# Kernel tuning notes

Hardware: AMD Instinct MI355X
Metric: run time of the kernel (lower is better)

The kernel has to match this reference:

```python
import jax, jax.numpy as jnp
import numpy as np
import math

B, S, DIM = 2, 2048, 1024
H, D = 16, 64  # num_head, head_dim; H*D == DIM

def setup_inputs() -> dict:
    key = jax.random.key(0)
    ks = jax.random.split(key, 10)
    s = 0.02
    return {
        "X": jax.random.normal(ks[0], (B, S, DIM), dtype=jnp.float32),
        "mask": jnp.ones((B, S), dtype=jnp.float32),
        "Wq": jax.random.normal(ks[1], (DIM, H * D), dtype=jnp.float32) * s,
        "bq": jnp.zeros((H * D,), dtype=jnp.float32),
        "Wk": jax.random.normal(ks[2], (DIM, H * D), dtype=jnp.float32) * s,
        "bk": jnp.zeros((H * D,), dtype=jnp.float32),
        "Wv": jax.random.normal(ks[3], (DIM, H * D), dtype=jnp.float32) * s,
        "bv": jnp.zeros((H * D,), dtype=jnp.float32),
        "Wo": jax.random.normal(ks[4], (H * D, DIM), dtype=jnp.float32) * s,
        "bo": jnp.zeros((DIM,), dtype=jnp.float32),
    }

def _split_heads(x):
    # [B, S, H*D] -> [B, H, S, D]
    b, s, _ = x.shape
    return x.reshape(b, s, H, D).transpose(0, 2, 1, 3)

def reference(X, mask, Wq, bq, Wk, bk, Wv, bv, Wo, bo):
    Q = _split_heads(X @ Wq + bq)
    K = _split_heads(X @ Wk + bk)
    V = _split_heads(X @ Wv + bv)
    # scaled dot-product attention with additive mask penalty
    dot = jnp.einsum('bhqd,bhkd->bhqk', Q, K) / math.sqrt(D)
    dot = dot - 1e6 * (1.0 - mask[:, None, None, :])
    attn = jax.nn.softmax(dot, axis=-1)
    ctx = jnp.einsum('bhqk,bhkd->bhqd', attn, V)
    # combine heads: [B, H, S, D] -> [B, S, H*D]
    ctx = ctx.transpose(0, 2, 1, 3).reshape(B, S, H * D)
    return ctx @ Wo + bo
```

## Files before the change

kernel.cpp:

```cpp
#include <hip/hip_runtime.h>
#include <cstdint>
#include <cstddef>

typedef __attribute__((ext_vector_type(8))) _Float16 f16x8;
typedef __attribute__((ext_vector_type(4))) _Float16 f16x4;
typedef __attribute__((ext_vector_type(4))) float f32x4;

#define MFMA_16x16x32(a, b, c) __builtin_amdgcn_mfma_f32_16x16x32_f16((a), (b), (c), 0, 0, 0)
#define MFMA_16x16x16(a, b, c) __builtin_amdgcn_mfma_f32_16x16x16f16((a), (b), (c), 0, 0, 0)

static constexpr int kB = 2, kS = 2048, kDim = 1024, kH = 16, kD = 64;
static constexpr int kM = kB * kS;
static constexpr float kQScale = 0.125f * 1.44269504088896340736f;
static constexpr float kPenC = 1.44269504088896340736e6f;

__device__ __forceinline__ void wg_barrier_lds() {
  asm volatile("s_waitcnt lgkmcnt(0)" ::: "memory");
  __builtin_amdgcn_s_barrier();
}

__global__ void cvt_f32_to_f16(const float* __restrict__ in, _Float16* __restrict__ out, int n8) {
  int i = blockIdx.x * blockDim.x + threadIdx.x;
  if (i >= n8) return;
  const float4* p = (const float4*)in + (size_t)i * 2;
  float4 a = p[0], b = p[1];
  f16x8 h;
  h[0] = (_Float16)a.x; h[1] = (_Float16)a.y; h[2] = (_Float16)a.z; h[3] = (_Float16)a.w;
  h[4] = (_Float16)b.x; h[5] = (_Float16)b.y; h[6] = (_Float16)b.z; h[7] = (_Float16)b.w;
  ((f16x8*)out)[i] = h;
}

__global__ void transpose_cvt_w(const float* __restrict__ w0, const float* __restrict__ w1,
                                const float* __restrict__ w2, const float* __restrict__ w3,
                                _Float16* __restrict__ o0, _Float16* __restrict__ o1,
                                _Float16* __restrict__ o2, _Float16* __restrict__ o3) {
  const float* w; _Float16* o;
  switch (blockIdx.z) {
    case 0: w = w0; o = o0; break;
    case 1: w = w1; o = o1; break;
    case 2: w = w2; o = o2; break;
    default: w = w3; o = o3; break;
  }
  __shared__ alignas(16) _Float16 tile[64][72];
  const int kt = blockIdx.x * 64;
  const int nt = blockIdx.y * 64;
  const int tr = threadIdx.x >> 4;
  const int tc = threadIdx.x & 15;
#pragma unroll
  for (int rr = 0; rr < 4; ++rr) {
    int r = rr * 16 + tr;
    float4 v = *(const float4*)&w[(size_t)(kt + r) * kDim + nt + tc * 4];
    f16x4 hv;
    hv[0] = (_Float16)v.x; hv[1] = (_Float16)v.y; hv[2] = (_Float16)v.z; hv[3] = (_Float16)v.w;
    *(f16x4*)&tile[r][tc * 4] = hv;
  }
  __syncthreads();
#pragma unroll
  for (int rr = 0; rr < 4; ++rr) {
    int nl = rr * 16 + tr;
    f16x4 hv;
    hv[0] = tile[tc * 4 + 0][nl];
    hv[1] = tile[tc * 4 + 1][nl];
    hv[2] = tile[tc * 4 + 2][nl];
    hv[3] = tile[tc * 4 + 3][nl];
    *(f16x4*)&o[(size_t)(nt + nl) * kDim + kt + tc * 4] = hv;
  }
}

__global__ __launch_bounds__(256, 3) void gemm_qkv(
    const _Float16* __restrict__ A,
    const _Float16* __restrict__ wt0, const _Float16* __restrict__ wt1, const _Float16* __restrict__ wt2,
    const float* __restrict__ bias0, const float* __restrict__ bias1, const float* __restrict__ bias2,
    _Float16* __restrict__ oq, _Float16* __restrict__ ok, _Float16* __restrict__ ov) {
  const _Float16* Bt; const float* bias; _Float16* out;
  switch (blockIdx.z) {
    case 0: Bt = wt0; bias = bias0; out = oq; break;
    case 1: Bt = wt1; bias = bias1; out = ok; break;
    default: Bt = wt2; bias = bias2; out = ov; break;
  }
  __shared__ alignas(16) _Float16 As[2][128 * 40];
  __shared__ alignas(16) _Float16 Bs[2][128 * 40];
  const int tid = threadIdx.x;
  const int lane = tid & 63;
  const int wave = tid >> 6;
  const int wm = wave & 1, wn = wave >> 1;
  const int l15 = lane & 15, quad = lane >> 4;
  const int m0 = blockIdx.x * 128, n0 = blockIdx.y * 128;

  const int srow = tid >> 2;
  const int skc = (tid & 3) * 8;

  f32x4 acc[4][4] = {};
  f16x8 ra[2], rb[2];

#pragma unroll
  for (int i = 0; i < 2; ++i) {
    int row = srow + 64 * i;
    ra[i] = *(const f16x8*)&A[(size_t)(m0 + row) * kDim + skc];
    rb[i] = *(const f16x8*)&Bt[(size_t)(n0 + row) * kDim + skc];
  }
#pragma unroll
  for (int i = 0; i < 2; ++i) {
    int row = srow + 64 * i;
    *(f16x8*)&As[0][row * 40 + skc] = ra[i];
    *(f16x8*)&Bs[0][row * 40 + skc] = rb[i];
  }

  for (int kt = 0; kt < 32; ++kt) {
    const int cur = kt & 1;
    if (kt + 1 < 32) {
      int k0 = (kt + 1) * 32;
#pragma unroll
      for (int i = 0; i < 2; ++i) {
        int row = srow + 64 * i;
        ra[i] = *(const f16x8*)&A[(size_t)(m0 + row) * kDim + k0 + skc];
        rb[i] = *(const f16x8*)&Bt[(size_t)(n0 + row) * kDim + k0 + skc];
      }
    }
    wg_barrier_lds();
    {
      f16x8 af[4], bf[4];
#pragma unroll
      for (int t = 0; t < 4; ++t) af[t] = *(const f16x8*)&As[cur][(wm * 64 + t * 16 + l15) * 40 + quad * 8];
#pragma unroll
      for (int t = 0; t < 4; ++t) bf[t] = *(const f16x8*)&Bs[cur][(wn * 64 + t * 16 + l15) * 40 + quad * 8];
      __builtin_amdgcn_s_setprio(1);
#pragma unroll
      for (int i = 0; i < 4; ++i)
#pragma unroll
        for (int j = 0; j < 4; ++j)
          acc[i][j] = MFMA_16x16x32(af[i], bf[j], acc[i][j]);
      __builtin_amdgcn_s_setprio(0);
    }
    if (kt + 1 < 32) {
#pragma unroll
      for (int i = 0; i < 2; ++i) {
        int row = srow + 64 * i;
        *(f16x8*)&As[cur ^ 1][row * 40 + skc] = ra[i];
        *(f16x8*)&Bs[cur ^ 1][row * 40 + skc] = rb[i];
      }
    }
  }

  const int mbase = m0 + wm * 64 + quad * 4;
  const int nbase = n0 + wn * 64 + l15;
  if (blockIdx.z == 2) {
#pragma unroll
    for (int j = 0; j < 4; ++j) {
      int n = nbase + j * 16;
      float bv = bias[n];
      int h = n >> 6, d = n & 63;
#pragma unroll
      for (int i = 0; i < 4; ++i) {
        int m = mbase + i * 16;
        int b = m >> 11, s = m & (kS - 1);
        f16x4 hv;
#pragma unroll
        for (int r = 0; r < 4; ++r) hv[r] = (_Float16)(acc[i][j][r] + bv);
        *(f16x4*)&out[((size_t)((b * kH + h) * kD + d)) * kS + s] = hv;
      }
    }
  } else {
    const float osc = (blockIdx.z == 0) ? kQScale : 1.0f;
#pragma unroll
    for (int j = 0; j < 4; ++j) {
      int n = nbase + j * 16;
      float bv = bias[n];
      int h = n >> 6, d = n & 63;
#pragma unroll
      for (int i = 0; i < 4; ++i) {
        int mrow = mbase + i * 16;
#pragma unroll
        for (int r = 0; r < 4; ++r) {
          int m = mrow + r;
          int b = m >> 11, s = m & (kS - 1);
          out[(size_t)(((b * kH + h) * kS) + s) * kD + d] = (_Float16)((acc[i][j][r] + bv) * osc);
        }
      }
    }
  }
}

__global__ __launch_bounds__(256, 2) void attn(
    const _Float16* __restrict__ Q, const _Float16* __restrict__ K,
    const _Float16* __restrict__ V, const float* __restrict__ mask,
    _Float16* __restrict__ ctx) {
  const int id = blockIdx.x;
  const int logical = (id & 7) * 64 + (id >> 3);
  const int bh = logical >> 4;
  const int qblk = logical & 15;
  const int b = bh >> 4;
  const int q0 = qblk * 128;
  const int tid = threadIdx.x, lane = tid & 63, wave = tid >> 6;
  const int l15 = lane & 15, quad = lane >> 4;

  __shared__ alignas(16) _Float16 Ks[2][128 * 72];
  __shared__ alignas(16) _Float16 Vs[2][64 * 136];
  __shared__ alignas(16) float pens[kS];

  const _Float16* Qh = Q + (size_t)bh * kS * kD;
  const _Float16* Kh = K + (size_t)bh * kS * kD;
  const _Float16* Vh = V + (size_t)bh * kS * kD;

#pragma unroll
  for (int i = 0; i < 2; ++i) {
    float4 mv4 = *(const float4*)&mask[(size_t)b * kS + tid * 8 + i * 4];
    float4 pv;
    pv.x = (mv4.x - 1.0f) * kPenC;
    pv.y = (mv4.y - 1.0f) * kPenC;
    pv.z = (mv4.z - 1.0f) * kPenC;
    pv.w = (mv4.w - 1.0f) * kPenC;
    *(float4*)&pens[tid * 8 + i * 4] = pv;
  }

  f16x8 qf[2][2];
#pragma unroll
  for (int t = 0; t < 2; ++t) {
    int qrow = q0 + wave * 32 + t * 16 + l15;
#pragma unroll
    for (int kk = 0; kk < 2; ++kk)
      qf[t][kk] = *(const f16x8*)&Qh[(size_t)qrow * kD + kk * 32 + quad * 8];
  }

  f16x4 ones4;
#pragma unroll
  for (int i = 0; i < 4; ++i) ones4[i] = (_Float16)1.0f;

  f32x4 o_acc[2][4] = {};
  f32x4 l_acc[2] = {};

  const int srow = tid >> 3;
  const int skc = (tid & 7) * 8;
  const int vrow = tid >> 4;
  const int vcol = (tid & 15) * 8;

  f16x8 kreg[4], vreg[4];
#pragma unroll
  for (int i = 0; i < 4; ++i)
    kreg[i] = *(const f16x8*)&Kh[(size_t)(srow + 32 * i) * kD + skc];
#pragma unroll
  for (int i = 0; i < 4; ++i)
    vreg[i] = *(const f16x8*)&Vh[(size_t)(vrow + 16 * i) * kS + vcol];
#pragma unroll
  for (int i = 0; i < 4; ++i)
    *(f16x8*)&Ks[0][(srow + 32 * i) * 72 + skc] = kreg[i];
#pragma unroll
  for (int i = 0; i < 4; ++i)
    *(f16x8*)&Vs[0][(vrow + 16 * i) * 136 + vcol] = vreg[i];

  for (int it = 0; it < 16; ++it) {
    const int cur = it & 1;
    const int kb = it * 128;
    if (it + 1 < 16) {
#pragma unroll
      for (int i = 0; i < 4; ++i)
        kreg[i] = *(const f16x8*)&Kh[(size_t)(kb + 128 + srow + 32 * i) * kD + skc];
#pragma unroll
      for (int i = 0; i < 4; ++i)
        vreg[i] = *(const f16x8*)&Vh[(size_t)(vrow + 16 * i) * kS + kb + 128 + vcol];
    }
    wg_barrier_lds();

#pragma unroll
    for (int colt = 0; colt < 8; ++colt) {
      f32x4 pn = *(const f32x4*)&pens[kb + colt * 16 + quad * 4];
      f16x8 kf0 = *(const f16x8*)&Ks[cur][(colt * 16 + l15) * 72 + quad * 8];
      f16x8 kf1 = *(const f16x8*)&Ks[cur][(colt * 16 + l15) * 72 + 32 + quad * 8];
      f32x4 s0 = pn, s1 = pn;
      s0 = MFMA_16x16x32(kf0, qf[0][0], s0);
      s0 = MFMA_16x16x32(kf1, qf[0][1], s0);
      s1 = MFMA_16x16x32(kf0, qf[1][0], s1);
      s1 = MFMA_16x16x32(kf1, qf[1][1], s1);
      f16x4 vf0 = *(const f16x4*)&Vs[cur][(0 * 16 + l15) * 136 + colt * 16 + quad * 4];
      f16x4 vf1 = *(const f16x4*)&Vs[cur][(1 * 16 + l15) * 136 + colt * 16 + quad * 4];
      f16x4 vf2 = *(const f16x4*)&Vs[cur][(2 * 16 + l15) * 136 + colt * 16 + quad * 4];
      f16x4 vf3 = *(const f16x4*)&Vs[cur][(3 * 16 + l15) * 136 + colt * 16 + quad * 4];
      f16x4 pa0, pa1;
#pragma unroll
      for (int r = 0; r < 4; ++r) {
        pa0[r] = (_Float16)__builtin_exp2f(s0[r]);
        pa1[r] = (_Float16)__builtin_exp2f(s1[r]);
      }
      __builtin_amdgcn_s_setprio(1);
      o_acc[0][0] = MFMA_16x16x16(pa0, vf0, o_acc[0][0]);
      o_acc[0][1] = MFMA_16x16x16(pa0, vf1, o_acc[0][1]);
      o_acc[0][2] = MFMA_16x16x16(pa0, vf2, o_acc[0][2]);
      o_acc[0][3] = MFMA_16x16x16(pa0, vf3, o_acc[0][3]);
      o_acc[1][0] = MFMA_16x16x16(pa1, vf0, o_acc[1][0]);
      o_acc[1][1] = MFMA_16x16x16(pa1, vf1, o_acc[1][1]);
      o_acc[1][2] = MFMA_16x16x16(pa1, vf2, o_acc[1][2]);
      o_acc[1][3] = MFMA_16x16x16(pa1, vf3, o_acc[1][3]);
      l_acc[0] = MFMA_16x16x16(pa0, ones4, l_acc[0]);
      l_acc[1] = MFMA_16x16x16(pa1, ones4, l_acc[1]);
      __builtin_amdgcn_s_setprio(0);
    }

    if (it + 1 < 16) {
#pragma unroll
      for (int i = 0; i < 4; ++i)
        *(f16x8*)&Ks[cur ^ 1][(srow + 32 * i) * 72 + skc] = kreg[i];
#pragma unroll
      for (int i = 0; i < 4; ++i)
        *(f16x8*)&Vs[cur ^ 1][(vrow + 16 * i) * 136 + vcol] = vreg[i];
    }
  }

  const int h = bh & 15;
#pragma unroll
  for (int t = 0; t < 2; ++t) {
    f32x4 linv;
#pragma unroll
    for (int r = 0; r < 4; ++r) linv[r] = 1.0f / l_acc[t][r];
    int qbase = q0 + wave * 32 + t * 16 + quad * 4;
#pragma unroll
    for (int c = 0; c < 4; ++c) {
#pragma unroll
      for (int r = 0; r < 4; ++r) {
        ctx[((size_t)(b * kS + qbase + r)) * kDim + h * kD + c * 16 + l15] =
            (_Float16)(o_acc[t][c][r] * linv[r]);
      }
    }
  }
}

__global__ __launch_bounds__(256, 2) void gemm_out(
    const _Float16* __restrict__ A, const _Float16* __restrict__ Bt,
    const float* __restrict__ bias, float* __restrict__ out) {
  __shared__ alignas(16) _Float16 As[2][64 * 72];
  __shared__ alignas(16) _Float16 Bs[2][128 * 72];
  const int tid = threadIdx.x;
  const int lane = tid & 63;
  const int wave = tid >> 6;
  const int wm = wave & 1, wn = wave >> 1;
  const int l15 = lane & 15, quad = lane >> 4;
  const int m0 = blockIdx.x * 64, n0 = blockIdx.y * 128;

  const int srow = tid >> 3;
  const int skc = (tid & 7) * 8;

  f32x4 acc[2][4] = {};
  f16x8 ra[2], rb[4];

#pragma unroll
  for (int i = 0; i < 2; ++i)
    ra[i] = *(const f16x8*)&A[(size_t)(m0 + srow + 32 * i) * kDim + skc];
#pragma unroll
  for (int i = 0; i < 4; ++i)
    rb[i] = *(const f16x8*)&Bt[(size_t)(n0 + srow + 32 * i) * kDim + skc];
#pragma unroll
  for (int i = 0; i < 2; ++i)
    *(f16x8*)&As[0][(srow + 32 * i) * 72 + skc] = ra[i];
#pragma unroll
  for (int i = 0; i < 4; ++i)
    *(f16x8*)&Bs[0][(srow + 32 * i) * 72 + skc] = rb[i];

  for (int kt = 0; kt < 16; ++kt) {
    const int cur = kt & 1;
    if (kt + 1 < 16) {
      int k0 = (kt + 1) * 64;
#pragma unroll
      for (int i = 0; i < 2; ++i)
        ra[i] = *(const f16x8*)&A[(size_t)(m0 + srow + 32 * i) * kDim + k0 + skc];
#pragma unroll
      for (int i = 0; i < 4; ++i)
        rb[i] = *(const f16x8*)&Bt[(size_t)(n0 + srow + 32 * i) * kDim + k0 + skc];
    }
    wg_barrier_lds();
#pragma unroll
    for (int kk = 0; kk < 2; ++kk) {
      f16x8 af[2], bf[4];
#pragma unroll
      for (int t = 0; t < 2; ++t) af[t] = *(const f16x8*)&As[cur][(wm * 32 + t * 16 + l15) * 72 + kk * 32 + quad * 8];
#pragma unroll
      for (int t = 0; t < 4; ++t) bf[t] = *(const f16x8*)&Bs[cur][(wn * 64 + t * 16 + l15) * 72 + kk * 32 + quad * 8];
      __builtin_amdgcn_s_setprio(1);
#pragma unroll
      for (int i = 0; i < 2; ++i)
#pragma unroll
        for (int j = 0; j < 4; ++j)
          acc[i][j] = MFMA_16x16x32(af[i], bf[j], acc[i][j]);
      __builtin_amdgcn_s_setprio(0);
    }
    if (kt + 1 < 16) {
#pragma unroll
      for (int i = 0; i < 2; ++i)
        *(f16x8*)&As[cur ^ 1][(srow + 32 * i) * 72 + skc] = ra[i];
#pragma unroll
      for (int i = 0; i < 4; ++i)
        *(f16x8*)&Bs[cur ^ 1][(srow + 32 * i) * 72 + skc] = rb[i];
    }
  }

  const int mbase = m0 + wm * 32 + quad * 4;
  const int nbase = n0 + wn * 64 + l15;
#pragma unroll
  for (int j = 0; j < 4; ++j) {
    int n = nbase + j * 16;
    float bv = bias[n];
#pragma unroll
    for (int i = 0; i < 2; ++i) {
      int mrow = mbase + i * 16;
#pragma unroll
      for (int r = 0; r < 4; ++r)
        out[(size_t)(mrow + r) * kDim + n] = acc[i][j][r] + bv;
    }
  }
}

extern "C" void kernel_launch(void* const* d_in, const int* in_sizes, int n_in,
                              void* d_out, int out_size, void* d_ws, size_t ws_size,
                              hipStream_t stream) {
  (void)in_sizes; (void)n_in; (void)out_size; (void)ws_size;
  const float* X    = (const float*)d_in[0];
  const float* mask = (const float*)d_in[1];
  const float* Wq   = (const float*)d_in[2];
  const float* bq   = (const float*)d_in[3];
  const float* Wk   = (const float*)d_in[4];
  const float* bk   = (const float*)d_in[5];
  const float* Wv   = (const float*)d_in[6];
  const float* bv   = (const float*)d_in[7];
  const float* Wo   = (const float*)d_in[8];
  const float* bo   = (const float*)d_in[9];
  float* out = (float*)d_out;

  char* ws = (char*)d_ws;
  _Float16* Xh   = (_Float16*)(ws);
  _Float16* Wqt  = (_Float16*)(ws + ((size_t)8  << 20));
  _Float16* Wkt  = (_Float16*)(ws + ((size_t)10 << 20));
  _Float16* Wvt  = (_Float16*)(ws + ((size_t)12 << 20));
  _Float16* Wot  = (_Float16*)(ws + ((size_t)14 << 20));
  _Float16* Qh   = (_Float16*)(ws + ((size_t)16 << 20));
  _Float16* Kh   = (_Float16*)(ws + ((size_t)24 << 20));
  _Float16* Vh   = (_Float16*)(ws + ((size_t)32 << 20));
  _Float16* Ch   = (_Float16*)(ws + ((size_t)40 << 20));

  cvt_f32_to_f16<<<dim3(kM * kDim / 8 / 256), dim3(256), 0, stream>>>(X, Xh, kM * kDim / 8);
  transpose_cvt_w<<<dim3(16, 16, 4), dim3(256), 0, stream>>>(Wq, Wk, Wv, Wo, Wqt, Wkt, Wvt, Wot);
  gemm_qkv<<<dim3(32, 8, 3), dim3(256), 0, stream>>>(Xh, Wqt, Wkt, Wvt, bq, bk, bv, Qh, Kh, Vh);
  attn<<<dim3(512), dim3(256), 0, stream>>>(Qh, Kh, Vh, mask, Ch);
  gemm_out<<<dim3(64, 8), dim3(256), 0, stream>>>(Ch, Wot, bo, out);
}
```

Measured before the change: 199.7 us.

## Use direct global-to-LDS loads with XOR swizzle in projection GEMMs

```diff
diff --git a/kernel.cpp b/kernel.cpp
--- a/kernel.cpp
+++ b/kernel.cpp
@@ -17,6 +17,14 @@
 __device__ __forceinline__ void wg_barrier_lds() {
   asm volatile("s_waitcnt lgkmcnt(0)" ::: "memory");
   __builtin_amdgcn_s_barrier();
+}
+__device__ __forceinline__ void wg_barrier_vm() {
+  asm volatile("s_waitcnt vmcnt(0) lgkmcnt(0)" ::: "memory");
+  __builtin_amdgcn_s_barrier();
+}
+__device__ __forceinline__ void gload16(const void* g, void* l) {
+  __builtin_amdgcn_global_load_lds((const __attribute__((address_space(1))) void*)g,
+                                   (__attribute__((address_space(3))) void*)l, 16, 0, 0);
 }
 
 __global__ void cvt_f32_to_f16(const float* __restrict__ in, _Float16* __restrict__ out, int n8) {
@@ -67,7 +75,7 @@
   }
 }
 
-__global__ __launch_bounds__(256, 3) void gemm_qkv(
+__global__ __launch_bounds__(256, 2) void gemm_qkv(
     const _Float16* __restrict__ A,
     const _Float16* __restrict__ wt0, const _Float16* __restrict__ wt1, const _Float16* __restrict__ wt2,
     const float* __restrict__ bias0, const float* __restrict__ bias1, const float* __restrict__ bias2,
@@ -78,8 +86,8 @@
     case 1: Bt = wt1; bias = bias1; out = ok; break;
     default: Bt = wt2; bias = bias2; out = ov; break;
   }
-  __shared__ alignas(16) _Float16 As[2][128 * 40];
-  __shared__ alignas(16) _Float16 Bs[2][128 * 40];
+  __shared__ alignas(16) _Float16 As[2][128 * 64];
+  __shared__ alignas(16) _Float16 Bs[2][128 * 64];
   const int tid = threadIdx.x;
   const int lane = tid & 63;
   const int wave = tid >> 6;
@@ -87,43 +95,43 @@
   const int l15 = lane & 15, quad = lane >> 4;
   const int m0 = blockIdx.x * 128, n0 = blockIdx.y * 128;
 
-  const int srow = tid >> 2;
-  const int skc = (tid & 3) * 8;
+  const int grow = lane >> 3;
+  const int gcol = ((lane & 7) ^ grow) * 8;
+  const _Float16* Asrc = A  + (size_t)(m0 + wave * 32 + grow) * kDim + gcol;
+  const _Float16* Bsrc = Bt + (size_t)(n0 + wave * 32 + grow) * kDim + gcol;
+
+  const int xr = l15 & 7;
+  const int slotA0 = ((quad) ^ xr) * 16, slotA1 = ((4 + quad) ^ xr) * 16;
+  const int rbaseA = (wm * 64 + l15) * 128;
+  const int rbaseB = (wn * 64 + l15) * 128;
 
   f32x4 acc[4][4] = {};
-  f16x8 ra[2], rb[2];
-
-#pragma unroll
-  for (int i = 0; i < 2; ++i) {
-    int row = srow + 64 * i;
-    ra[i] = *(const f16x8*)&A[(size_t)(m0 + row) * kDim + skc];
-    rb[i] = *(const f16x8*)&Bt[(size_t)(n0 + row) * kDim + skc];
-  }
-#pragma unroll
-  for (int i = 0; i < 2; ++i) {
-    int row = srow + 64 * i;
-    *(f16x8*)&As[0][row * 40 + skc] = ra[i];
-    *(f16x8*)&Bs[0][row * 40 + skc] = rb[i];
-  }
-
-  for (int kt = 0; kt < 32; ++kt) {
+
+#pragma unroll
+  for (int g = 0; g < 4; ++g) {
+    gload16(Asrc + (size_t)g * 8 * kDim, (char*)&As[0][0] + (wave * 32 + g * 8) * 128);
+    gload16(Bsrc + (size_t)g * 8 * kDim, (char*)&Bs[0][0] + (wave * 32 + g * 8) * 128);
+  }
+  wg_barrier_vm();
+
+  for (int kt = 0; kt < 16; ++kt) {
     const int cur = kt & 1;
-    if (kt + 1 < 32) {
-      int k0 = (kt + 1) * 32;
-#pragma unroll
-      for (int i = 0; i < 2; ++i) {
-        int row = srow + 64 * i;
-        ra[i] = *(const f16x8*)&A[(size_t)(m0 + row) * kDim + k0 + skc];
-        rb[i] = *(const f16x8*)&Bt[(size_t)(n0 + row) * kDim + k0 + skc];
+    if (kt + 1 < 16) {
+      int koff = (kt + 1) * 64;
+#pragma unroll
+      for (int g = 0; g < 4; ++g) {
+        gload16(Asrc + (size_t)g * 8 * kDim + koff, (char*)&As[cur ^ 1][0] + (wave * 32 + g * 8) * 128);
+        gload16(Bsrc + (size_t)g * 8 * kDim + koff, (char*)&Bs[cur ^ 1][0] + (wave * 32 + g * 8) * 128);
       }
     }
-    wg_barrier_lds();
-    {
+#pragma unroll
+    for (int kk = 0; kk < 2; ++kk) {
+      const int sa = kk ? slotA1 : slotA0;
       f16x8 af[4], bf[4];
 #pragma unroll
-      for (int t = 0; t < 4; ++t) af[t] = *(const f16x8*)&As[cur][(wm * 64 + t * 16 + l15) * 40 + quad * 8];
-#pragma unroll
-      for (int t = 0; t < 4; ++t) bf[t] = *(const f16x8*)&Bs[cur][(wn * 64 + t * 16 + l15) * 40 + quad * 8];
+      for (int t = 0; t < 4; ++t) af[t] = *(const f16x8*)((const char*)&As[cur][0] + rbaseA + t * 2048 + sa);
+#pragma unroll
+      for (int t = 0; t < 4; ++t) bf[t] = *(const f16x8*)((const char*)&Bs[cur][0] + rbaseB + t * 2048 + sa);
       __builtin_amdgcn_s_setprio(1);
 #pragma unroll
       for (int i = 0; i < 4; ++i)
@@ -132,14 +140,7 @@
           acc[i][j] = MFMA_16x16x32(af[i], bf[j], acc[i][j]);
       __builtin_amdgcn_s_setprio(0);
     }
-    if (kt + 1 < 32) {
-#pragma unroll
-      for (int i = 0; i < 2; ++i) {
-        int row = srow + 64 * i;
-        *(f16x8*)&As[cur ^ 1][row * 40 + skc] = ra[i];
-        *(f16x8*)&Bs[cur ^ 1][row * 40 + skc] = rb[i];
-      }
-    }
+    if (kt + 1 < 16) wg_barrier_vm();
   }
 
   const int mbase = m0 + wm * 64 + quad * 4;
@@ -326,8 +327,8 @@
 __global__ __launch_bounds__(256, 2) void gemm_out(
     const _Float16* __restrict__ A, const _Float16* __restrict__ Bt,
     const float* __restrict__ bias, float* __restrict__ out) {
-  __shared__ alignas(16) _Float16 As[2][64 * 72];
-  __shared__ alignas(16) _Float16 Bs[2][128 * 72];
+  __shared__ alignas(16) _Float16 As[2][64 * 64];
+  __shared__ alignas(16) _Float16 Bs[2][128 * 64];
   const int tid = threadIdx.x;
   const int lane = tid & 63;
   const int wave = tid >> 6;
@@ -335,44 +336,45 @@
   const int l15 = lane & 15, quad = lane >> 4;
   const int m0 = blockIdx.x * 64, n0 = blockIdx.y * 128;
 
-  const int srow = tid >> 3;
-  const int skc = (tid & 7) * 8;
+  const int grow = lane >> 3;
+  const int gcol = ((lane & 7) ^ grow) * 8;
+  const _Float16* Asrc = A  + (size_t)(m0 + wave * 16 + grow) * kDim + gcol;
+  const _Float16* Bsrc = Bt + (size_t)(n0 + wave * 32 + grow) * kDim + gcol;
+
+  const int xr = l15 & 7;
+  const int slot0 = ((quad) ^ xr) * 16, slot1 = ((4 + quad) ^ xr) * 16;
+  const int rbaseA = (wm * 32 + l15) * 128;
+  const int rbaseB = (wn * 64 + l15) * 128;
 
   f32x4 acc[2][4] = {};
-  f16x8 ra[2], rb[4];
-
-#pragma unroll
-  for (int i = 0; i < 2; ++i)
-    ra[i] = *(const f16x8*)&A[(size_t)(m0 + srow + 32 * i) * kDim + skc];
-#pragma unroll
-  for (int i = 0; i < 4; ++i)
-    rb[i] = *(const f16x8*)&Bt[(size_t)(n0 + srow + 32 * i) * kDim + skc];
-#pragma unroll
-  for (int i = 0; i < 2; ++i)
-    *(f16x8*)&As[0][(srow + 32 * i) * 72 + skc] = ra[i];
-#pragma unroll
-  for (int i = 0; i < 4; ++i)
-    *(f16x8*)&Bs[0][(srow + 32 * i) * 72 + skc] = rb[i];
+
+#pragma unroll
+  for (int g = 0; g < 2; ++g)
+    gload16(Asrc + (size_t)g * 8 * kDim, (char*)&As[0][0] + (wave * 16 + g * 8) * 128);
+#pragma unroll
+  for (int g = 0; g < 4; ++g)
+    gload16(Bsrc + (size_t)g * 8 * kDim, (char*)&Bs[0][0] + (wave * 32 + g * 8) * 128);
+  wg_barrier_vm();
 
   for (int kt = 0; kt < 16; ++kt) {
     const int cur = kt & 1;
     if (kt + 1 < 16) {
-      int k0 = (kt + 1) * 64;
-#pragma unroll
-      for (int i = 0; i < 2; ++i)
-        ra[i] = *(const f16x8*)&A[(size_t)(m0 + srow + 32 * i) * kDim + k0 + skc];
-#pragma unroll
-      for (int i = 0; i < 4; ++i)
-        rb[i] = *(const f16x8*)&Bt[(size_t)(n0 + srow + 32 * i) * kDim + k0 + skc];
-    }
-    wg_barrier_lds();
+      int koff = (kt + 1) * 64;
+#pragma unroll
+      for (int g = 0; g < 2; ++g)
+        gload16(Asrc + (size_t)g * 8 * kDim + koff, (char*)&As[cur ^ 1][0] + (wave * 16 + g * 8) * 128);
+#pragma unroll
+      for (int g = 0; g < 4; ++g)
+        gload16(Bsrc + (size_t)g * 8 * kDim + koff, (char*)&Bs[cur ^ 1][0] + (wave * 32 + g * 8) * 128);
+    }
 #pragma unroll
     for (int kk = 0; kk < 2; ++kk) {
+      const int sa = kk ? slot1 : slot0;
       f16x8 af[2], bf[4];
 #pragma unroll
-      for (int t = 0; t < 2; ++t) af[t] = *(const f16x8*)&As[cur][(wm * 32 + t * 16 + l15) * 72 + kk * 32 + quad * 8];
-#pragma unroll
-      for (int t = 0; t < 4; ++t) bf[t] = *(const f16x8*)&Bs[cur][(wn * 64 + t * 16 + l15) * 72 + kk * 32 + quad * 8];
+      for (int t = 0; t < 2; ++t) af[t] = *(const f16x8*)((const char*)&As[cur][0] + rbaseA + t * 2048 + sa);
+#pragma unroll
+      for (int t = 0; t < 4; ++t) bf[t] = *(const f16x8*)((const char*)&Bs[cur][0] + rbaseB + t * 2048 + sa);
       __builtin_amdgcn_s_setprio(1);
 #pragma unroll
       for (int i = 0; i < 2; ++i)
@@ -381,14 +383,7 @@
           acc[i][j] = MFMA_16x16x32(af[i], bf[j], acc[i][j]);
       __builtin_amdgcn_s_setprio(0);
     }
-    if (kt + 1 < 16) {
-#pragma unroll
-      for (int i = 0; i < 2; ++i)
-        *(f16x8*)&As[cur ^ 1][(srow + 32 * i) * 72 + skc] = ra[i];
-#pragma unroll
-      for (int i = 0; i < 4; ++i)
-        *(f16x8*)&Bs[cur ^ 1][(srow + 32 * i) * 72 + skc] = rb[i];
-    }
+    if (kt + 1 < 16) wg_barrier_vm();
   }
 
   const int mbase = m0 + wm * 32 + quad * 4;
```

New measurement: 204.8 us. 2.6% more time.
